# Performance work log

Hardware: AMD Instinct MI355X
Metric: run time of the kernel (lower is better)

## Reference

```python
import jax, jax.numpy as jnp
import numpy as np

N, E, R, H = 50000, 400000, 3, 3
IN, HID, OUT, C, B = 128, 64, 64, 16, 8


def _deg_norm(idx):
    # DGL GraphConv norm='both': deg.clamp(min=1) ** -0.5
    deg = jax.ops.segment_sum(jnp.ones(idx.shape, jnp.float32), idx, N)
    return jnp.maximum(deg, 1.0) ** -0.5


def _graph_conv(h, W, b, s, d):
    # h: [N, ..., F_in]; norm by src out-degree, matmul, scatter-sum to dst, norm by dst in-degree
    ns, nd = _deg_norm(s), _deg_norm(d)
    bshape = (N,) + (1,) * (h.ndim - 1)
    hw = (h * ns.reshape(bshape)) @ W
    agg = jax.ops.segment_sum(hw[s], d, N)
    return agg * nd.reshape(bshape) + b


def _gat(h, W, al, ar, b, s, d):
    # h: [N, HID] -> [N, H, HID] multi-head GAT with edge softmax over incoming edges
    f = (h @ W).reshape(N, H, HID)
    el = jnp.sum(f * al, axis=-1)  # [N, H]
    er = jnp.sum(f * ar, axis=-1)  # [N, H]
    e = jax.nn.leaky_relu(el[s] + er[d], 0.2)  # [E, H]
    m = jax.ops.segment_max(e, d, N)
    ez = jnp.exp(e - m[d])
    z = jax.ops.segment_sum(ez, d, N)
    alpha = ez / (z[d] + 1e-9)  # [E, H]
    out = jax.ops.segment_sum(alpha[:, :, None] * f[s], d, N)  # [N, H, HID]
    return out + b.reshape(H, HID)


def setup_inputs() -> dict:
    key = jax.random.key(0)
    k = jax.random.split(key, 12)
    s = 0.05
    return {
        "x": jax.random.normal(k[0], (N, IN), jnp.float32),
        "src": jax.random.randint(k[1], (R, E), 0, N, jnp.int32),
        "dst": jax.random.randint(k[2], (R, E), 0, N, jnp.int32),
        "graph_id": (jnp.arange(N, dtype=jnp.int32) * B // N).astype(jnp.int32),
        "W1": jax.random.normal(k[3], (R, IN, HID), jnp.float32) * s,
        "b1": jnp.zeros((R, HID), jnp.float32),
        "Wg": jax.random.normal(k[4], (R, HID, H * HID), jnp.float32) * s,
        "al": jax.random.normal(k[5], (R, H, HID), jnp.float32) * s,
        "ar": jax.random.normal(k[6], (R, H, HID), jnp.float32) * s,
        "bg": jnp.zeros((R, H * HID), jnp.float32),
        "W2": jax.random.normal(k[7], (R, HID, OUT), jnp.float32) * s,
        "b2": jnp.zeros((R, OUT), jnp.float32),
        "Wc": jax.random.normal(k[8], (OUT, C), jnp.float32) * s,
        "bc": jnp.zeros((C,), jnp.float32),
    }


def reference(x, src, dst, graph_id, W1, b1, Wg, al, ar, bg, W2, b2, Wc, bc):
    # conv1: per-relation GraphConv, aggregate='sum'
    h = sum(_graph_conv(x, W1[r], b1[r], src[r], dst[r]) for r in range(R))  # [N, HID]
    # F.normalize (L2 over dim=1, eps=1e-12)
    h = h / jnp.maximum(jnp.linalg.norm(h, axis=1, keepdims=True), 1e-12)
    # gatconv: per-relation GAT (3 heads), aggregate='sum'
    h = sum(_gat(h, Wg[r], al[r], ar[r], bg[r], src[r], dst[r]) for r in range(R))  # [N, H, HID]
    h = jax.nn.relu(h)
    # dropout(0.3) omitted: deterministic eval reference
    # conv2: GraphConv applied per head
    h = sum(_graph_conv(h, W2[r], b2[r], src[r], dst[r]) for r in range(R))  # [N, H, OUT]
    h = jax.nn.sigmoid(h)
    # dgl.mean_nodes over batched graphs
    cnt = jax.ops.segment_sum(jnp.ones((N,), jnp.float32), graph_id, B)
    pooled = jax.ops.segment_sum(h, graph_id, B) / jnp.maximum(cnt, 1.0)[:, None, None]  # [B, H, OUT]
    hg = jax.nn.sigmoid(pooled @ Wc + bc)  # [B, H, C]
    return jnp.mean(hg, axis=2)  # [B, H]
```

## Files before the change

kernel.cpp:

```cpp
#include <hip/hip_runtime.h>
#include <math.h>

#define NN 50000
#define EE 400000
#define RR 3
#define NH 3
#define FIN 128
#define HID 64
#define FOUT 64
#define NC 16
#define NB 8
#define NGAT 208

#define NBLK 32
#define CHK (EE / NBLK)
#define NRNG 4
#define RNGSZ (NN / NRNG)

typedef __attribute__((ext_vector_type(8))) short v8s;
typedef __attribute__((ext_vector_type(4))) float v4f;
typedef unsigned short u16;
typedef unsigned char u8;
typedef unsigned int u32;
typedef __attribute__((ext_vector_type(4))) unsigned short u16x4;

#define QS 32.0f
#define IQS (1.0f / 32.0f)

__device__ __forceinline__ u16 f2b(float f) {
  unsigned u = __float_as_uint(f);
  return (u16)((u + 0x7fffu + ((u >> 16) & 1u)) >> 16);
}
__device__ __forceinline__ float b2f(u16 b) {
  return __uint_as_float(((unsigned)b) << 16);
}
__device__ __forceinline__ float wexp(float e) {
  e = e > 0.f ? e : 0.2f * e;
  return __expf(e);
}
__device__ __forceinline__ u8 f2e(float v) {
  return (u8)(__builtin_amdgcn_cvt_pk_fp8_f32(v, 0.f, 0, false) & 0xff);
}

__global__ __launch_bounds__(1024) void k_hist(const int* __restrict__ src,
                                               const int* __restrict__ dst,
                                               u16* __restrict__ ps,
                                               u16* __restrict__ pd,
                                               u16* __restrict__ rank) {
  __shared__ u32 h[RNGSZ];
  int b = blockIdx.x;
  int kind = blockIdx.y >> 2, range = blockIdx.y & 3;
  int r = blockIdx.z;
  int lo = range * RNGSZ;
  for (int i = threadIdx.x; i < RNGSZ; i += 1024) h[i] = 0;
  __syncthreads();
  int base = r * EE + b * CHK;
  if (kind) {
    for (int i = threadIdx.x; i < CHK; i += 1024) {
      int d = dst[base + i] - lo;
      if ((unsigned)d < RNGSZ) rank[base + i] = (u16)atomicAdd(&h[d], 1u);
    }
  } else {
    for (int i = threadIdx.x; i < CHK; i += 1024) {
      int s = src[base + i] - lo;
      if ((unsigned)s < RNGSZ) atomicAdd(&h[s], 1u);
    }
  }
  __syncthreads();
  u16* p = (kind ? pd : ps) + (size_t)(r * NBLK + b) * NN + lo;
  for (int i = threadIdx.x; i < RNGSZ; i += 1024) p[i] = (u16)h[i];
}

__global__ void k_red(const u16* __restrict__ ps, const u16* __restrict__ pd,
                      int* __restrict__ degd, float* __restrict__ ns,
                      float* __restrict__ nd, u16* __restrict__ bpfx) {
  int i = blockIdx.x * 256 + threadIdx.x;
  if (i >= RR * NN) return;
  int r = i / NN, n = i - r * NN;
  u32 ss = 0, sd = 0;
  for (int b = 0; b < NBLK; ++b) {
    size_t o = (size_t)(r * NBLK + b) * NN + n;
    ss += ps[o];
    bpfx[o] = (u16)sd;
    sd += pd[o];
  }
  degd[i] = (int)sd;
  ns[i] = 1.0f / sqrtf((float)(ss > 1 ? ss : 1));
  nd[i] = 1.0f / sqrtf((float)(sd > 1 ? sd : 1));
}

__global__ void k_scan1(const int* __restrict__ deg, int* __restrict__ offs,
                        int* __restrict__ bsum) {
  __shared__ int sh[256];
  int gid = blockIdx.x * 256 + threadIdx.x;
  int v = (gid < RR * NN) ? deg[gid] : 0;
  sh[threadIdx.x] = v;
  __syncthreads();
  for (int off = 1; off < 256; off <<= 1) {
    int t = (threadIdx.x >= off) ? sh[threadIdx.x - off] : 0;
    __syncthreads();
    sh[threadIdx.x] += t;
    __syncthreads();
  }
  if (gid < RR * NN) offs[gid] = sh[threadIdx.x] - v;
  if (threadIdx.x == 255) bsum[blockIdx.x] = sh[255];
}

__global__ void k_scan2(int* __restrict__ bsum, int nb) {
  __shared__ int sh[1024];
  int v = (threadIdx.x < nb) ? bsum[threadIdx.x] : 0;
  sh[threadIdx.x] = v;
  __syncthreads();
  for (int off = 1; off < 1024; off <<= 1) {
    int t = (threadIdx.x >= off) ? sh[threadIdx.x - off] : 0;
    __syncthreads();
    sh[threadIdx.x] += t;
    __syncthreads();
  }
  if (threadIdx.x < nb) bsum[threadIdx.x] = sh[threadIdx.x] - v;
}

__global__ void k_scan3(int* __restrict__ offs, const int* __restrict__ bsum) {
  int i = blockIdx.x * 256 + threadIdx.x;
  if (i >= RR * NN) return;
  offs[i] = offs[i] + bsum[i / 256];
}

__global__ __launch_bounds__(1024) void k_place(const int* __restrict__ src,
                                                const int* __restrict__ dst,
                                                const int* __restrict__ offs,
                                                const u16* __restrict__ bpfx,
                                                const u16* __restrict__ rank,
                                                int* __restrict__ esrc) {
  int b = blockIdx.x;
  int range = blockIdx.y;
  int r = blockIdx.z;
  int lo = range * RNGSZ;
  int base = r * EE + b * CHK;
  for (int i = threadIdx.x; i < CHK; i += 1024) {
    int d = dst[base + i] - lo;
    if ((unsigned)d < RNGSZ) {
      int dg = d + lo;
      size_t o = (size_t)(r * NBLK + b) * NN + dg;
      int pos = offs[r * NN + dg] + (int)bpfx[o] + (int)rank[base + i];
      esrc[pos] = src[base + i];
    }
  }
}

__global__ void k_cast(const float4* __restrict__ in, u16x4* __restrict__ out, int n4) {
  int i = blockIdx.x * 256 + threadIdx.x;
  if (i >= n4) return;
  float4 v = in[i];
  u16x4 o;
  o.x = f2b(v.x); o.y = f2b(v.y); o.z = f2b(v.z); o.w = f2b(v.w);
  out[i] = o;
}

__global__ void k_bcomp(const float* __restrict__ Wg, const float* __restrict__ al,
                        const float* __restrict__ ar, float* __restrict__ B) {
  int i = blockIdx.x * 256 + threadIdx.x;
  if (i >= RR * HID * NGAT) return;
  int col = i % NGAT;
  int k = (i / NGAT) % HID;
  int r = i / (NGAT * HID);
  float v = 0.f;
  if (col < NH * HID) {
    v = Wg[((size_t)(r * HID + k)) * (NH * HID) + col];
  } else if (col < NH * HID + 6) {
    int c2 = col - NH * HID;
    int isar = c2 / NH, h = c2 % NH;
    const float* wg = Wg + ((size_t)(r * HID + k)) * (NH * HID) + h * HID;
    const float* av = (isar ? ar : al) + (r * NH + h) * HID;
    float a = 0.f;
#pragma unroll 8
    for (int c = 0; c < HID; ++c) a += wg[c] * av[c];
    v = a;
  }
  B[i] = v;
}

template <int K, int N, int OUTMODE>
__global__ __launch_bounds__(256) void k_gemm(const u16* __restrict__ A, int lda,
                                              const float* __restrict__ B0, int bstr,
                                              void* __restrict__ C0,
                                              u16* __restrict__ elr,
                                              const float* __restrict__ s0, int M) {
  constexpr int KP = K + 8;
  __shared__ __align__(16) u16 Bt[N * KP];
  int y = blockIdx.y;
  int rrel = (OUTMODE == 3) ? y / NH : y;
  int head = (OUTMODE == 3) ? y % NH : 0;
  const float* B = B0 + (size_t)rrel * bstr;
  const float* scale = s0 + (size_t)rrel * NN;
  const u16* Ab = A + head * HID;
  for (int i = threadIdx.x; i < K * N; i += 256) {
    int k = i / N, n = i % N;
    Bt[n * KP + k] = f2b(B[(size_t)k * N + n]);
  }
  __syncthreads();
  int wid = threadIdx.x >> 6, lane = threadIdx.x & 63;
  int l15 = lane & 15, lg = lane >> 4;
  constexpr int NT = N / 16;
  int ntiles = (M + 63) >> 6;
  for (int tile = blockIdx.x; tile < ntiles; tile += gridDim.x) {
    int mbase = tile * 64 + wid * 16;
    v4f acc[NT];
#pragma unroll
    for (int t = 0; t < NT; ++t) acc[t] = (v4f)(0.f);
    int arow = mbase + l15;
    if (arow >= M) arow = M - 1;
    const u16* ap = Ab + (size_t)arow * lda + lg * 8;
#pragma unroll
    for (int ks = 0; ks < K / 32; ++ks) {
      v8s a = *(const v8s*)(ap + ks * 32);
#pragma unroll
      for (int t = 0; t < NT; ++t) {
        v8s b = *(const v8s*)(&Bt[(t * 16 + l15) * KP + lg * 8 + ks * 32]);
        acc[t] = __builtin_amdgcn_mfma_f32_16x16x32_bf16(a, b, acc[t], 0, 0, 0);
      }
    }
#pragma unroll
    for (int q = 0; q < 4; ++q) {
      int row = mbase + lg * 4 + q;
      if (row >= M) continue;
      if (OUTMODE == 1) {
        float s = scale[row] * QS;
        u8* C = (u8*)C0 + ((size_t)y * M + row) * 64;
#pragma unroll
        for (int t = 0; t < NT; ++t) C[t * 16 + l15] = f2e(acc[t][q] * s);
      } else if (OUTMODE == 2) {
        u32* C = (u32*)C0 + ((size_t)y * M + row) * 64;
#pragma unroll
        for (int tm = 0; tm < 4; ++tm) {
          u32 pk = __builtin_amdgcn_cvt_pk_fp8_f32(acc[tm][q] * QS,
                                                   acc[tm + 4][q] * QS, 0, false);
          pk = __builtin_amdgcn_cvt_pk_fp8_f32(acc[tm + 8][q] * QS, 0.f, pk, true);
          C[tm * 16 + l15] = pk;
        }
        if (l15 < 6)
          elr[((size_t)y * M + row) * 8 + (l15 < 3 ? l15 : l15 + 1)] =
              f2b(acc[12][q]);
      } else {
        float s = scale[row] * QS;
        u8* C = (u8*)C0 + (((size_t)rrel * M + row) * 64) * 4 + head;
#pragma unroll
        for (int t = 0; t < NT; ++t) C[(t * 16 + l15) * 4] = f2e(acc[t][q] * s);
      }
    }
  }
}

__global__ void k_g1(const int* __restrict__ offs, const int* __restrict__ degd,
                     const int* __restrict__ esrc, const u8* __restrict__ c1pk,
                     const float* __restrict__ nd, const float* __restrict__ b1,
                     u16* __restrict__ h1b) {
  int node = blockIdx.x * 4 + (threadIdx.x >> 6);
  int lane = threadIdx.x & 63;
  if (node >= NN) return;
  float v = 0.f;
#pragma unroll
  for (int r = 0; r < RR; ++r) {
    int start = offs[r * NN + node];
    int deg = degd[r * NN + node];
    const u8* base = c1pk + (size_t)r * NN * 64 + lane;
    float t = 0.f;
    int j = 0;
    for (; j + 4 <= deg; j += 4) {
      int s0 = esrc[start + j], s1 = esrc[start + j + 1];
      int s2 = esrc[start + j + 2], s3 = esrc[start + j + 3];
      float a0 = __builtin_amdgcn_cvt_f32_fp8((u32)base[(size_t)s0 * 64], 0);
      float a1 = __builtin_amdgcn_cvt_f32_fp8((u32)base[(size_t)s1 * 64], 0);
      float a2 = __builtin_amdgcn_cvt_f32_fp8((u32)base[(size_t)s2 * 64], 0);
      float a3 = __builtin_amdgcn_cvt_f32_fp8((u32)base[(size_t)s3 * 64], 0);
      t += (a0 + a1) + (a2 + a3);
    }
    for (; j < deg; ++j)
      t += __builtin_amdgcn_cvt_f32_fp8((u32)base[(size_t)esrc[start + j] * 64], 0);
    v += t * nd[r * NN + node];
  }
  v = v * IQS + b1[lane] + b1[HID + lane] + b1[2 * HID + lane];
  float sq = v * v;
  for (int off = 32; off; off >>= 1) sq += __shfl_xor(sq, off);
  float nrm = sqrtf(sq);
  nrm = nrm > 1e-12f ? nrm : 1e-12f;
  h1b[node * HID + lane] = f2b(v / nrm);
}

__global__ void k_ew(const int* __restrict__ offs, const int* __restrict__ degd,
                     const int* __restrict__ esrc, const u16* __restrict__ elr,
                     u16* __restrict__ ew) {
  int i = blockIdx.x * 256 + threadIdx.x;
  if (i >= RR * NN) return;
  int r = i / NN;
  int start = offs[i], deg = degd[i];
  const u16* ed = elr + (size_t)i * 8 + 4;
  float e0 = b2f(ed[0]), e1 = b2f(ed[1]), e2 = b2f(ed[2]);
  for (int j = 0; j < deg; ++j) {
    int s = esrc[start + j];
    const u16* es = elr + ((size_t)r * NN + s) * 8;
    u16x4 o;
    o.x = f2b(wexp(b2f(es[0]) + e0));
    o.y = f2b(wexp(b2f(es[1]) + e1));
    o.z = f2b(wexp(b2f(es[2]) + e2));
    o.w = 0;
    *(u16x4*)(ew + (size_t)(start + j) * 4) = o;
  }
}

__global__ void k_gatg(const int* __restrict__ offs, const int* __restrict__ degd,
                       const int* __restrict__ esrc, const u32* __restrict__ fpk,
                       const u16* __restrict__ ew, const float* __restrict__ bg,
                       u16* __restrict__ gatb) {
  int node = blockIdx.x * 4 + (threadIdx.x >> 6);
  int lane = threadIdx.x & 63;
  if (node >= NN) return;
  float o0 = 0.f, o1 = 0.f, o2 = 0.f;
#pragma unroll
  for (int r = 0; r < RR; ++r) {
    const u32* f = fpk + (size_t)r * NN * 64 + lane;
    int start = offs[r * NN + node];
    int deg = degd[r * NN + node];
    float z0 = 0.f, z1 = 0.f, z2 = 0.f;
    float a0 = 0.f, a1 = 0.f, a2 = 0.f;
    int j = 0;
    for (; j + 4 <= deg; j += 4) {
      int p = start + j;
      int s0 = esrc[p], s1 = esrc[p + 1], s2 = esrc[p + 2], s3 = esrc[p + 3];
      u16x4 wa = *(const u16x4*)(ew + (size_t)p * 4);
      u16x4 wb = *(const u16x4*)(ew + (size_t)(p + 1) * 4);
      u16x4 wc = *(const u16x4*)(ew + (size_t)(p + 2) * 4);
      u16x4 wd = *(const u16x4*)(ew + (size_t)(p + 3) * 4);
      u32 v0 = f[(size_t)s0 * 64];
      u32 v1 = f[(size_t)s1 * 64];
      u32 v2 = f[(size_t)s2 * 64];
      u32 v3 = f[(size_t)s3 * 64];
      float w;
      w = b2f(wa.x); z0 += w; a0 += w * __builtin_amdgcn_cvt_f32_fp8(v0, 0);
      w = b2f(wa.y); z1 += w; a1 += w * __builtin_amdgcn_cvt_f32_fp8(v0, 1);
      w = b2f(wa.z); z2 += w; a2 += w * __builtin_amdgcn_cvt_f32_fp8(v0, 2);
      w = b2f(wb.x); z0 += w; a0 += w * __builtin_amdgcn_cvt_f32_fp8(v1, 0);
      w = b2f(wb.y); z1 += w; a1 += w * __builtin_amdgcn_cvt_f32_fp8(v1, 1);
      w = b2f(wb.z); z2 += w; a2 += w * __builtin_amdgcn_cvt_f32_fp8(v1, 2);
      w = b2f(wc.x); z0 += w; a0 += w * __builtin_amdgcn_cvt_f32_fp8(v2, 0);
      w = b2f(wc.y); z1 += w; a1 += w * __builtin_amdgcn_cvt_f32_fp8(v2, 1);
      w = b2f(wc.z); z2 += w; a2 += w * __builtin_amdgcn_cvt_f32_fp8(v2, 2);
      w = b2f(wd.x); z0 += w; a0 += w * __builtin_amdgcn_cvt_f32_fp8(v3, 0);
      w = b2f(wd.y); z1 += w; a1 += w * __builtin_amdgcn_cvt_f32_fp8(v3, 1);
      w = b2f(wd.z); z2 += w; a2 += w * __builtin_amdgcn_cvt_f32_fp8(v3, 2);
    }
    for (; j < deg; ++j) {
      int p = start + j;
      u16x4 wa = *(const u16x4*)(ew + (size_t)p * 4);
      u32 v0 = f[(size_t)esrc[p] * 64];
      float w;
      w = b2f(wa.x); z0 += w; a0 += w * __builtin_amdgcn_cvt_f32_fp8(v0, 0);
      w = b2f(wa.y); z1 += w; a1 += w * __builtin_amdgcn_cvt_f32_fp8(v0, 1);
      w = b2f(wa.z); z2 += w; a2 += w * __builtin_amdgcn_cvt_f32_fp8(v0, 2);
    }
    o0 += a0 / (z0 + 1e-9f);
    o1 += a1 / (z1 + 1e-9f);
    o2 += a2 / (z2 + 1e-9f);
  }
  float ov[NH] = {o0, o1, o2};
#pragma unroll
  for (int h = 0; h < NH; ++h) {
    int j = h * HID + lane;
    float v = ov[h] * IQS + bg[j] + bg[NH * HID + j] + bg[2 * NH * HID + j];
    gatb[(size_t)node * (NH * HID) + j] = f2b(fmaxf(v, 0.f));
  }
}

__global__ void k_g2(const int* __restrict__ offs, const int* __restrict__ degd,
                     const int* __restrict__ esrc, const u32* __restrict__ c2pk,
                     const float* __restrict__ nd, const float* __restrict__ b2,
                     u16* __restrict__ agg2b) {
  int node = blockIdx.x * 4 + (threadIdx.x >> 6);
  int lane = threadIdx.x & 63;
  if (node >= NN) return;
  float o0 = 0.f, o1 = 0.f, o2 = 0.f;
#pragma unroll
  for (int r = 0; r < RR; ++r) {
    const u32* hw = c2pk + (size_t)r * NN * 64 + lane;
    int start = offs[r * NN + node];
    int deg = degd[r * NN + node];
    float a0 = 0.f, a1 = 0.f, a2 = 0.f;
    int j = 0;
    for (; j + 4 <= deg; j += 4) {
      int p = start + j;
      u32 v0 = hw[(size_t)esrc[p] * 64];
      u32 v1 = hw[(size_t)esrc[p + 1] * 64];
      u32 v2 = hw[(size_t)esrc[p + 2] * 64];
      u32 v3 = hw[(size_t)esrc[p + 3] * 64];
      a0 += (__builtin_amdgcn_cvt_f32_fp8(v0, 0) + __builtin_amdgcn_cvt_f32_fp8(v1, 0)) +
            (__builtin_amdgcn_cvt_f32_fp8(v2, 0) + __builtin_amdgcn_cvt_f32_fp8(v3, 0));
      a1 += (__builtin_amdgcn_cvt_f32_fp8(v0, 1) + __builtin_amdgcn_cvt_f32_fp8(v1, 1)) +
            (__builtin_amdgcn_cvt_f32_fp8(v2, 1) + __builtin_amdgcn_cvt_f32_fp8(v3, 1));
      a2 += (__builtin_amdgcn_cvt_f32_fp8(v0, 2) + __builtin_amdgcn_cvt_f32_fp8(v1, 2)) +
            (__builtin_amdgcn_cvt_f32_fp8(v2, 2) + __builtin_amdgcn_cvt_f32_fp8(v3, 2));
    }
    for (; j < deg; ++j) {
      u32 v0 = hw[(size_t)esrc[start + j] * 64];
      a0 += __builtin_amdgcn_cvt_f32_fp8(v0, 0);
      a1 += __builtin_amdgcn_cvt_f32_fp8(v0, 1);
      a2 += __builtin_amdgcn_cvt_f32_fp8(v0, 2);
    }
    float ndv = nd[r * NN + node];
    o0 += a0 * ndv; o1 += a1 * ndv; o2 += a2 * ndv;
  }
  float b2s = b2[lane] + b2[FOUT + lane] + b2[2 * FOUT + lane];
  float ov[NH] = {o0, o1, o2};
#pragma unroll
  for (int h = 0; h < NH; ++h) {
    float v = 1.0f / (1.0f + __expf(-(ov[h] * IQS + b2s)));
    agg2b[(size_t)node * (NH * FOUT) + h * FOUT + lane] = f2b(v);
  }
}

__global__ void k_cnt2(const int* __restrict__ gid, float* __restrict__ cnt) {
  __shared__ int loc[NB];
  if (threadIdx.x < NB) loc[threadIdx.x] = 0;
  __syncthreads();
  int i = blockIdx.x * 256 + threadIdx.x;
  if (i < NN) atomicAdd(&loc[gid[i]], 1);
  __syncthreads();
  if (threadIdx.x < NB) atomicAdd(&cnt[threadIdx.x], (float)loc[threadIdx.x]);
}

__global__ void k_pool(const u16* __restrict__ h3, const int* __restrict__ gid,
                       float* __restrict__ pooled) {
  int j = threadIdx.x;
  int start = blockIdx.x * 128;
  if (start >= NN) return;
  int end = start + 128;
  if (end > NN) end = NN;
  int gcur = gid[start];
  float acc = 0.f;
  for (int n = start; n < end; ++n) {
    int g = gid[n];
    if (g != gcur) {
      atomicAdd(&pooled[gcur * (NH * FOUT) + j], acc);
      acc = 0.f;
      gcur = g;
    }
    acc += b2f(h3[(size_t)n * (NH * FOUT) + j]);
  }
  atomicAdd(&pooled[gcur * (NH * FOUT) + j], acc);
}

__global__ void k_final(const float* __restrict__ pooled, const float* __restrict__ cnt,
                        const float* __restrict__ Wc, const float* __restrict__ bc,
                        float* __restrict__ out) {
  int t = threadIdx.x;
  if (t >= NB * NH) return;
  int b = t / NH;
  float inv = 1.0f / fmaxf(cnt[b], 1.0f);
  const float* p = pooled + t * FOUT;
  float sacc = 0.f;
  for (int c = 0; c < NC; ++c) {
    float acc = bc[c];
    for (int o = 0; o < FOUT; ++o) acc += p[o] * inv * Wc[o * NC + c];
    sacc += 1.0f / (1.0f + __expf(-acc));
  }
  out[t] = sacc * (1.0f / NC);
}

extern "C" void kernel_launch(void* const* d_in, const int* in_sizes, int n_in,
                              void* d_out, int out_size, void* d_ws, size_t ws_size,
                              hipStream_t stream) {
  const float* x = (const float*)d_in[0];
  const int* src = (const int*)d_in[1];
  const int* dst = (const int*)d_in[2];
  const int* gid = (const int*)d_in[3];
  const float* W1 = (const float*)d_in[4];
  const float* b1 = (const float*)d_in[5];
  const float* Wg = (const float*)d_in[6];
  const float* al = (const float*)d_in[7];
  const float* ar = (const float*)d_in[8];
  const float* bg = (const float*)d_in[9];
  const float* W2 = (const float*)d_in[10];
  const float* b2 = (const float*)d_in[11];
  const float* Wc = (const float*)d_in[12];
  const float* bc = (const float*)d_in[13];
  float* out = (float*)d_out;

  float* cnt = (float*)d_ws;
  float* pooled = cnt + NB;
  size_t zero_bytes = ((size_t)NB + NB * NH * FOUT) * 4;
  int* degd = (int*)(pooled + NB * NH * FOUT);
  int* offs = degd + RR * NN;
  int* bsum = offs + RR * NN + 8;
  int* esrc = bsum + 1024;
  float* ns = (float*)(esrc + (size_t)RR * EE);
  float* nd = ns + RR * NN;
  float* Bcomp = nd + RR * NN;
  u16* elr = (u16*)(Bcomp + RR * HID * NGAT);
  u16* ew = elr + (size_t)RR * NN * 8;
  u16* xb = ew + (size_t)RR * EE * 4;
  u16* h1b = xb + (size_t)NN * FIN;
  u8* c1pk = (u8*)(h1b + (size_t)NN * HID);
  u16* gatb = (u16*)(c1pk + (size_t)RR * NN * 64);
  u32* fpk = (u32*)(gatb + (size_t)NN * NH * HID);
  u32* c2pk = fpk;
  u16* agg2b = xb;
  u16* ps = (u16*)fpk;
  u16* pd = ps + (size_t)RR * NBLK * NN;
  u16* bpfx = pd + (size_t)RR * NBLK * NN;
  u16* rank = bpfx + (size_t)RR * NBLK * NN;

  hipMemsetAsync(d_ws, 0, zero_bytes, stream);

  const int nscan = RR * NN;
  const int nblk1 = (nscan + 255) / 256;

  k_hist<<<dim3(NBLK, 8, RR), 1024, 0, stream>>>(src, dst, ps, pd, rank);
  k_red<<<nblk1, 256, 0, stream>>>(ps, pd, degd, ns, nd, bpfx);
  k_scan1<<<nblk1, 256, 0, stream>>>(degd, offs, bsum);
  k_scan2<<<1, 1024, 0, stream>>>(bsum, nblk1);
  k_scan3<<<nblk1, 256, 0, stream>>>(offs, bsum);
  k_place<<<dim3(NBLK, NRNG, RR), 1024, 0, stream>>>(src, dst, offs, bpfx, rank, esrc);

  k_cast<<<(NN * FIN / 4 + 255) / 256, 256, 0, stream>>>((const float4*)x, (u16x4*)xb,
                                                         NN * FIN / 4);
  k_bcomp<<<(RR * HID * NGAT + 255) / 256, 256, 0, stream>>>(Wg, al, ar, Bcomp);

  k_gemm<FIN, HID, 1><<<dim3(782, RR), 256, 0, stream>>>(
      xb, FIN, W1, FIN * HID, c1pk, nullptr, ns, NN);
  k_g1<<<(NN + 3) / 4, 256, 0, stream>>>(offs, degd, esrc, c1pk, nd, b1, h1b);

  k_gemm<HID, NGAT, 2><<<dim3(782, RR), 256, 0, stream>>>(
      h1b, HID, Bcomp, HID * NGAT, fpk, elr, ns, NN);
  k_ew<<<nblk1, 256, 0, stream>>>(offs, degd, esrc, elr, ew);
  k_gatg<<<(NN + 3) / 4, 256, 0, stream>>>(offs, degd, esrc, fpk, ew, bg, gatb);

  k_gemm<HID, FOUT, 3><<<dim3(782, RR * NH), 256, 0, stream>>>(
      gatb, NH * HID, W2, HID * FOUT, c2pk, nullptr, ns, NN);
  k_g2<<<(NN + 3) / 4, 256, 0, stream>>>(offs, degd, esrc, c2pk, nd, b2, agg2b);

  k_cnt2<<<(NN + 255) / 256, 256, 0, stream>>>(gid, cnt);
  k_pool<<<(NN + 127) / 128, 192, 0, stream>>>(agg2b, gid, pooled);
  k_final<<<1, 64, 0, stream>>>(pooled, cnt, Wc, bc, out);
}
```

Before: 552.8 us.

## Reorder GAT and conv2 to aggregate before matmul, stacking relations into one GEMM

The GAT layer now gathers the 64-wide normalized features (fp8) per edge, weighted by softmax coefficients normalized in a separate edge pass. The head projection then runs afterwards as a single GEMM over stacked per-relation aggregates (K=192). conv2 likewise aggregates the 64-wide per-head features before one stacked GEMM, with bias and sigmoid fused into its epilogue. This cuts gather width and removes the large per-relation GAT projection. In exchange it adds a second exp pass over edges and a larger intermediate aggregate buffer that is written and then read back by the GEMMs.

```diff
diff --git a/kernel.cpp b/kernel.cpp
--- a/kernel.cpp
+++ b/kernel.cpp
@@ -10,7 +10,6 @@
 #define FOUT 64
 #define NC 16
 #define NB 8
-#define NGAT 208
 
 #define NBLK 32
 #define CHK (EE / NBLK)
@@ -157,19 +156,16 @@
   out[i] = o;
 }
 
-__global__ void k_bcomp(const float* __restrict__ Wg, const float* __restrict__ al,
-                        const float* __restrict__ ar, float* __restrict__ B) {
-  int i = blockIdx.x * 256 + threadIdx.x;
-  if (i >= RR * HID * NGAT) return;
-  int col = i % NGAT;
-  int k = (i / NGAT) % HID;
-  int r = i / (NGAT * HID);
+__global__ void k_wel(const float* __restrict__ Wg, const float* __restrict__ al,
+                      const float* __restrict__ ar, float* __restrict__ Bel) {
+  int i = blockIdx.x * 256 + threadIdx.x;
+  if (i >= RR * HID * 16) return;
+  int col = i & 15;
+  int k = (i >> 4) % HID;
+  int r = i / (16 * HID);
   float v = 0.f;
-  if (col < NH * HID) {
-    v = Wg[((size_t)(r * HID + k)) * (NH * HID) + col];
-  } else if (col < NH * HID + 6) {
-    int c2 = col - NH * HID;
-    int isar = c2 / NH, h = c2 % NH;
+  if (col < 6) {
+    int isar = col / 3, h = col % 3;
     const float* wg = Wg + ((size_t)(r * HID + k)) * (NH * HID) + h * HID;
     const float* av = (isar ? ar : al) + (r * NH + h) * HID;
     float a = 0.f;
@@ -177,23 +173,48 @@
     for (int c = 0; c < HID; ++c) a += wg[c] * av[c];
     v = a;
   }
-  B[i] = v;
+  Bel[i] = v;
+}
+
+__global__ void k_wstack(const float* __restrict__ Wg, const float* __restrict__ W2,
+                         const float* __restrict__ bg, const float* __restrict__ b2,
+                         float* __restrict__ Bg, float* __restrict__ B2s,
+                         float* __restrict__ bgs, float* __restrict__ b2s) {
+  int i = blockIdx.x * 256 + threadIdx.x;
+  const int NG = RR * 192 * 64;
+  const int N2 = 192 * 64;
+  if (i < NG) {
+    int o = i & 63;
+    int rk = (i >> 6) % 192;
+    int h = i / (192 * 64);
+    int r = rk >> 6, k = rk & 63;
+    Bg[i] = Wg[((size_t)(r * HID + k)) * (NH * HID) + h * HID + o];
+  } else if (i < NG + N2) {
+    int j = i - NG;
+    int o = j & 63;
+    int rk = j >> 6;
+    int r = rk >> 6, k = rk & 63;
+    B2s[j] = W2[((size_t)(r * HID + k)) * FOUT + o];
+  } else if (i < NG + N2 + 192) {
+    int j = i - NG - N2;
+    bgs[j] = bg[j] + bg[192 + j] + bg[384 + j];
+  } else if (i < NG + N2 + 192 + 64) {
+    int j = i - NG - N2 - 192;
+    b2s[j] = b2[j] + b2[64 + j] + b2[128 + j];
+  }
 }
 
 template <int K, int N, int OUTMODE>
 __global__ __launch_bounds__(256) void k_gemm(const u16* __restrict__ A, int lda,
                                               const float* __restrict__ B0, int bstr,
                                               void* __restrict__ C0,
-                                              u16* __restrict__ elr,
+                                              const float* __restrict__ bias,
                                               const float* __restrict__ s0, int M) {
   constexpr int KP = K + 8;
   __shared__ __align__(16) u16 Bt[N * KP];
   int y = blockIdx.y;
-  int rrel = (OUTMODE == 3) ? y / NH : y;
-  int head = (OUTMODE == 3) ? y % NH : 0;
-  const float* B = B0 + (size_t)rrel * bstr;
-  const float* scale = s0 + (size_t)rrel * NN;
-  const u16* Ab = A + head * HID;
+  const float* B = B0 + (size_t)y * bstr;
+  const u16* Ab = (OUTMODE == 5 || OUTMODE == 6) ? A + y * 192 : A;
   for (int i = threadIdx.x; i < K * N; i += 256) {
     int k = i / N, n = i % N;
     Bt[n * KP + k] = f2b(B[(size_t)k * N + n]);
@@ -225,27 +246,28 @@
       int row = mbase + lg * 4 + q;
       if (row >= M) continue;
       if (OUTMODE == 1) {
-        float s = scale[row] * QS;
+        float s = s0[(size_t)y * NN + row] * QS;
         u8* C = (u8*)C0 + ((size_t)y * M + row) * 64;
 #pragma unroll
         for (int t = 0; t < NT; ++t) C[t * 16 + l15] = f2e(acc[t][q] * s);
-      } else if (OUTMODE == 2) {
-        u32* C = (u32*)C0 + ((size_t)y * M + row) * 64;
-#pragma unroll
-        for (int tm = 0; tm < 4; ++tm) {
-          u32 pk = __builtin_amdgcn_cvt_pk_fp8_f32(acc[tm][q] * QS,
-                                                   acc[tm + 4][q] * QS, 0, false);
-          pk = __builtin_amdgcn_cvt_pk_fp8_f32(acc[tm + 8][q] * QS, 0.f, pk, true);
-          C[tm * 16 + l15] = pk;
+      } else if (OUTMODE == 4) {
+        if (l15 < 6)
+          ((u16*)C0)[((size_t)y * M + row) * 8 + (l15 < 3 ? l15 : l15 + 1)] =
+              f2b(acc[0][q]);
+      } else if (OUTMODE == 5) {
+        u8* C = (u8*)C0 + (size_t)row * 192 + y * 64;
+#pragma unroll
+        for (int t = 0; t < NT; ++t) {
+          float v = acc[t][q] * IQS + bias[y * 64 + t * 16 + l15];
+          C[t * 16 + l15] = f2e(fmaxf(v, 0.f) * QS);
         }
-        if (l15 < 6)
-          elr[((size_t)y * M + row) * 8 + (l15 < 3 ? l15 : l15 + 1)] =
-              f2b(acc[12][q]);
       } else {
-        float s = scale[row] * QS;
-        u8* C = (u8*)C0 + (((size_t)rrel * M + row) * 64) * 4 + head;
-#pragma unroll
-        for (int t = 0; t < NT; ++t) C[(t * 16 + l15) * 4] = f2e(acc[t][q] * s);
+        u16* C = (u16*)C0 + (size_t)row * 192 + y * 64;
+#pragma unroll
+        for (int t = 0; t < NT; ++t) {
+          float v = acc[t][q] * IQS + bias[t * 16 + l15];
+          C[t * 16 + l15] = f2b(1.0f / (1.0f + __expf(-v)));
+        }
       }
     }
   }
@@ -254,7 +276,7 @@
 __global__ void k_g1(const int* __restrict__ offs, const int* __restrict__ degd,
                      const int* __restrict__ esrc, const u8* __restrict__ c1pk,
                      const float* __restrict__ nd, const float* __restrict__ b1,
-                     u16* __restrict__ h1b) {
+                     u16* __restrict__ h1b, u8* __restrict__ h1q) {
   int node = blockIdx.x * 4 + (threadIdx.x >> 6);
   int lane = threadIdx.x & 63;
   if (node >= NN) return;
@@ -284,44 +306,52 @@
   for (int off = 32; off; off >>= 1) sq += __shfl_xor(sq, off);
   float nrm = sqrtf(sq);
   nrm = nrm > 1e-12f ? nrm : 1e-12f;
-  h1b[node * HID + lane] = f2b(v / nrm);
-}
-
-__global__ void k_ew(const int* __restrict__ offs, const int* __restrict__ degd,
-                     const int* __restrict__ esrc, const u16* __restrict__ elr,
-                     u16* __restrict__ ew) {
+  float hv = v / nrm;
+  h1b[node * HID + lane] = f2b(hv);
+  h1q[node * HID + lane] = f2e(hv * QS);
+}
+
+__global__ void k_ew2(const int* __restrict__ offs, const int* __restrict__ degd,
+                      const int* __restrict__ esrc, const u16* __restrict__ elr,
+                      u16* __restrict__ ew) {
   int i = blockIdx.x * 256 + threadIdx.x;
   if (i >= RR * NN) return;
   int r = i / NN;
   int start = offs[i], deg = degd[i];
   const u16* ed = elr + (size_t)i * 8 + 4;
   float e0 = b2f(ed[0]), e1 = b2f(ed[1]), e2 = b2f(ed[2]);
+  float z0 = 0.f, z1 = 0.f, z2 = 0.f;
+  for (int j = 0; j < deg; ++j) {
+    int s = esrc[start + j];
+    const u16* es = elr + ((size_t)r * NN + s) * 8;
+    z0 += wexp(b2f(es[0]) + e0);
+    z1 += wexp(b2f(es[1]) + e1);
+    z2 += wexp(b2f(es[2]) + e2);
+  }
+  float i0 = 1.f / (z0 + 1e-9f), i1 = 1.f / (z1 + 1e-9f), i2 = 1.f / (z2 + 1e-9f);
   for (int j = 0; j < deg; ++j) {
     int s = esrc[start + j];
     const u16* es = elr + ((size_t)r * NN + s) * 8;
     u16x4 o;
-    o.x = f2b(wexp(b2f(es[0]) + e0));
-    o.y = f2b(wexp(b2f(es[1]) + e1));
-    o.z = f2b(wexp(b2f(es[2]) + e2));
+    o.x = f2b(wexp(b2f(es[0]) + e0) * i0);
+    o.y = f2b(wexp(b2f(es[1]) + e1) * i1);
+    o.z = f2b(wexp(b2f(es[2]) + e2) * i2);
     o.w = 0;
     *(u16x4*)(ew + (size_t)(start + j) * 4) = o;
   }
 }
 
-__global__ void k_gatg(const int* __restrict__ offs, const int* __restrict__ degd,
-                       const int* __restrict__ esrc, const u32* __restrict__ fpk,
-                       const u16* __restrict__ ew, const float* __restrict__ bg,
-                       u16* __restrict__ gatb) {
+__global__ void k_gatg2(const int* __restrict__ offs, const int* __restrict__ degd,
+                        const int* __restrict__ esrc, const u8* __restrict__ h1q,
+                        const u16* __restrict__ ew, u16* __restrict__ agg) {
   int node = blockIdx.x * 4 + (threadIdx.x >> 6);
   int lane = threadIdx.x & 63;
   if (node >= NN) return;
-  float o0 = 0.f, o1 = 0.f, o2 = 0.f;
+  const u8* base = h1q + lane;
 #pragma unroll
   for (int r = 0; r < RR; ++r) {
-    const u32* f = fpk + (size_t)r * NN * 64 + lane;
     int start = offs[r * NN + node];
     int deg = degd[r * NN + node];
-    float z0 = 0.f, z1 = 0.f, z2 = 0.f;
     float a0 = 0.f, a1 = 0.f, a2 = 0.f;
     int j = 0;
     for (; j + 4 <= deg; j += 4) {
@@ -331,89 +361,70 @@
       u16x4 wb = *(const u16x4*)(ew + (size_t)(p + 1) * 4);
       u16x4 wc = *(const u16x4*)(ew + (size_t)(p + 2) * 4);
       u16x4 wd = *(const u16x4*)(ew + (size_t)(p + 3) * 4);
-      u32 v0 = f[(size_t)s0 * 64];
-      u32 v1 = f[(size_t)s1 * 64];
-      u32 v2 = f[(size_t)s2 * 64];
-      u32 v3 = f[(size_t)s3 * 64];
-      float w;
-      w = b2f(wa.x); z0 += w; a0 += w * __builtin_amdgcn_cvt_f32_fp8(v0, 0);
-      w = b2f(wa.y); z1 += w; a1 += w * __builtin_amdgcn_cvt_f32_fp8(v0, 1);
-      w = b2f(wa.z); z2 += w; a2 += w * __builtin_amdgcn_cvt_f32_fp8(v0, 2);
-      w = b2f(wb.x); z0 += w; a0 += w * __builtin_amdgcn_cvt_f32_fp8(v1, 0);
-      w = b2f(wb.y); z1 += w; a1 += w * __builtin_amdgcn_cvt_f32_fp8(v1, 1);
-      w = b2f(wb.z); z2 += w; a2 += w * __builtin_amdgcn_cvt_f32_fp8(v1, 2);
-      w = b2f(wc.x); z0 += w; a0 += w * __builtin_amdgcn_cvt_f32_fp8(v2, 0);
-      w = b2f(wc.y); z1 += w; a1 += w * __builtin_amdgcn_cvt_f32_fp8(v2, 1);
-      w = b2f(wc.z); z2 += w; a2 += w * __builtin_amdgcn_cvt_f32_fp8(v2, 2);
-      w = b2f(wd.x); z0 += w; a0 += w * __builtin_amdgcn_cvt_f32_fp8(v3, 0);
-      w = b2f(wd.y); z1 += w; a1 += w * __builtin_amdgcn_cvt_f32_fp8(v3, 1);
-      w = b2f(wd.z); z2 += w; a2 += w * __builtin_amdgcn_cvt_f32_fp8(v3, 2);
+      float v0 = __builtin_amdgcn_cvt_f32_fp8((u32)base[(size_t)s0 * 64], 0);
+      float v1 = __builtin_amdgcn_cvt_f32_fp8((u32)base[(size_t)s1 * 64], 0);
+      float v2 = __builtin_amdgcn_cvt_f32_fp8((u32)base[(size_t)s2 * 64], 0);
+      float v3 = __builtin_amdgcn_cvt_f32_fp8((u32)base[(size_t)s3 * 64], 0);
+      a0 += b2f(wa.x) * v0 + b2f(wb.x) * v1 + b2f(wc.x) * v2 + b2f(wd.x) * v3;
+      a1 += b2f(wa.y) * v0 + b2f(wb.y) * v1 + b2f(wc.y) * v2 + b2f(wd.y) * v3;
+      a2 += b2f(wa.z) * v0 + b2f(wb.z) * v1 + b2f(wc.z) * v2 + b2f(wd.z) * v3;
     }
     for (; j < deg; ++j) {
       int p = start + j;
       u16x4 wa = *(const u16x4*)(ew + (size_t)p * 4);
-      u32 v0 = f[(size_t)esrc[p] * 64];
-      float w;
-      w = b2f(wa.x); z0 += w; a0 += w * __builtin_amdgcn_cvt_f32_fp8(v0, 0);
-      w = b2f(wa.y); z1 += w; a1 += w * __builtin_amdgcn_cvt_f32_fp8(v0, 1);
-      w = b2f(wa.z); z2 += w; a2 += w * __builtin_amdgcn_cvt_f32_fp8(v0, 2);
-    }
-    o0 += a0 / (z0 + 1e-9f);
-    o1 += a1 / (z1 + 1e-9f);
-    o2 += a2 / (z2 + 1e-9f);
-  }
-  float ov[NH] = {o0, o1, o2};
-#pragma unroll
-  for (int h = 0; h < NH; ++h) {
-    int j = h * HID + lane;
-    float v = ov[h] * IQS + bg[j] + bg[NH * HID + j] + bg[2 * NH * HID + j];
-    gatb[(size_t)node * (NH * HID) + j] = f2b(fmaxf(v, 0.f));
-  }
-}
-
-__global__ void k_g2(const int* __restrict__ offs, const int* __restrict__ degd,
-                     const int* __restrict__ esrc, const u32* __restrict__ c2pk,
-                     const float* __restrict__ nd, const float* __restrict__ b2,
-                     u16* __restrict__ agg2b) {
+      float v = __builtin_amdgcn_cvt_f32_fp8((u32)base[(size_t)esrc[p] * 64], 0);
+      a0 += b2f(wa.x) * v;
+      a1 += b2f(wa.y) * v;
+      a2 += b2f(wa.z) * v;
+    }
+    size_t ob = (size_t)node * 576 + r * 64 + lane;
+    agg[ob] = f2b(a0);
+    agg[ob + 192] = f2b(a1);
+    agg[ob + 384] = f2b(a2);
+  }
+}
+
+__global__ void k_g22(const int* __restrict__ offs, const int* __restrict__ degd,
+                      const int* __restrict__ esrc, const u8* __restrict__ gq,
+                      const float* __restrict__ ns, const float* __restrict__ nd,
+                      u16* __restrict__ agg) {
   int node = blockIdx.x * 4 + (threadIdx.x >> 6);
   int lane = threadIdx.x & 63;
   if (node >= NN) return;
-  float o0 = 0.f, o1 = 0.f, o2 = 0.f;
+  const u8* g0 = gq + lane;
+  const u8* g1 = gq + 64 + lane;
+  const u8* g2 = gq + 128 + lane;
 #pragma unroll
   for (int r = 0; r < RR; ++r) {
-    const u32* hw = c2pk + (size_t)r * NN * 64 + lane;
     int start = offs[r * NN + node];
     int deg = degd[r * NN + node];
+    const float* nsr = ns + (size_t)r * NN;
     float a0 = 0.f, a1 = 0.f, a2 = 0.f;
     int j = 0;
-    for (; j + 4 <= deg; j += 4) {
-      int p = start + j;
-      u32 v0 = hw[(size_t)esrc[p] * 64];
-      u32 v1 = hw[(size_t)esrc[p + 1] * 64];
-      u32 v2 = hw[(size_t)esrc[p + 2] * 64];
-      u32 v3 = hw[(size_t)esrc[p + 3] * 64];
-      a0 += (__builtin_amdgcn_cvt_f32_fp8(v0, 0) + __builtin_amdgcn_cvt_f32_fp8(v1, 0)) +
-            (__builtin_amdgcn_cvt_f32_fp8(v2, 0) + __builtin_amdgcn_cvt_f32_fp8(v3, 0));
-      a1 += (__builtin_amdgcn_cvt_f32_fp8(v0, 1) + __builtin_amdgcn_cvt_f32_fp8(v1, 1)) +
-            (__builtin_amdgcn_cvt_f32_fp8(v2, 1) + __builtin_amdgcn_cvt_f32_fp8(v3, 1));
-      a2 += (__builtin_amdgcn_cvt_f32_fp8(v0, 2) + __builtin_amdgcn_cvt_f32_fp8(v1, 2)) +
-            (__builtin_amdgcn_cvt_f32_fp8(v2, 2) + __builtin_amdgcn_cvt_f32_fp8(v3, 2));
-    }
-    for (; j < deg; ++j) {
-      u32 v0 = hw[(size_t)esrc[start + j] * 64];
-      a0 += __builtin_amdgcn_cvt_f32_fp8(v0, 0);
-      a1 += __builtin_amdgcn_cvt_f32_fp8(v0, 1);
-      a2 += __builtin_amdgcn_cvt_f32_fp8(v0, 2);
+    for (; j + 2 <= deg; j += 2) {
+      int s0 = esrc[start + j], s1 = esrc[start + j + 1];
+      float w0 = nsr[s0], w1 = nsr[s1];
+      size_t o0 = (size_t)s0 * 192, o1 = (size_t)s1 * 192;
+      a0 += w0 * __builtin_amdgcn_cvt_f32_fp8((u32)g0[o0], 0) +
+            w1 * __builtin_amdgcn_cvt_f32_fp8((u32)g0[o1], 0);
+      a1 += w0 * __builtin_amdgcn_cvt_f32_fp8((u32)g1[o0], 0) +
+            w1 * __builtin_amdgcn_cvt_f32_fp8((u32)g1[o1], 0);
+      a2 += w0 * __builtin_amdgcn_cvt_f32_fp8((u32)g2[o0], 0) +
+            w1 * __builtin_amdgcn_cvt_f32_fp8((u32)g2[o1], 0);
+    }
+    if (j < deg) {
+      int s0 = esrc[start + j];
+      float w0 = nsr[s0];
+      size_t o0 = (size_t)s0 * 192;
+      a0 += w0 * __builtin_amdgcn_cvt_f32_fp8((u32)g0[o0], 0);
+      a1 += w0 * __builtin_amdgcn_cvt_f32_fp8((u32)g1[o0], 0);
+      a2 += w0 * __builtin_amdgcn_cvt_f32_fp8((u32)g2[o0], 0);
     }
     float ndv = nd[r * NN + node];
-    o0 += a0 * ndv; o1 += a1 * ndv; o2 += a2 * ndv;
-  }
-  float b2s = b2[lane] + b2[FOUT + lane] + b2[2 * FOUT + lane];
-  float ov[NH] = {o0, o1, o2};
-#pragma unroll
-  for (int h = 0; h < NH; ++h) {
-    float v = 1.0f / (1.0f + __expf(-(ov[h] * IQS + b2s)));
-    agg2b[(size_t)node * (NH * FOUT) + h * FOUT + lane] = f2b(v);
+    size_t ob = (size_t)node * 576 + r * 64 + lane;
+    agg[ob] = f2b(a0 * ndv);
+    agg[ob + 192] = f2b(a1 * ndv);
+    agg[ob + 384] = f2b(a2 * ndv);
   }
 }
 
@@ -493,17 +504,21 @@
   int* esrc = bsum + 1024;
   float* ns = (float*)(esrc + (size_t)RR * EE);
   float* nd = ns + RR * NN;
-  float* Bcomp = nd + RR * NN;
-  u16* elr = (u16*)(Bcomp + RR * HID * NGAT);
+  float* Bel = nd + RR * NN;
+  float* Bg = Bel + RR * HID * 16;
+  float* B2s = Bg + RR * 192 * 64;
+  float* bgs = B2s + 192 * 64;
+  float* b2s = bgs + 192;
+  u16* elr = (u16*)(b2s + 64);
   u16* ew = elr + (size_t)RR * NN * 8;
   u16* xb = ew + (size_t)RR * EE * 4;
   u16* h1b = xb + (size_t)NN * FIN;
-  u8* c1pk = (u8*)(h1b + (size_t)NN * HID);
-  u16* gatb = (u16*)(c1pk + (size_t)RR * NN * 64);
-  u32* fpk = (u32*)(gatb + (size_t)NN * NH * HID);
-  u32* c2pk = fpk;
+  u8* h1q = (u8*)(h1b + (size_t)NN * HID);
+  u8* c1pk = h1q + (size_t)NN * HID;
+  u8* gq = c1pk + (size_t)RR * NN * 64;
+  u16* agg = (u16*)(gq + (size_t)NN * 192);
   u16* agg2b = xb;
-  u16* ps = (u16*)fpk;
+  u16* ps = agg;
   u16* pd = ps + (size_t)RR * NBLK * NN;
   u16* bpfx = pd + (size_t)RR * NBLK * NN;
   u16* rank = bpfx + (size_t)RR * NBLK * NN;
@@ -522,20 +537,24 @@
 
   k_cast<<<(NN * FIN / 4 + 255) / 256, 256, 0, stream>>>((const float4*)x, (u16x4*)xb,
                                                          NN * FIN / 4);
-  k_bcomp<<<(RR * HID * NGAT + 255) / 256, 256, 0, stream>>>(Wg, al, ar, Bcomp);
+  k_wel<<<(RR * HID * 16 + 255) / 256, 256, 0, stream>>>(Wg, al, ar, Bel);
+  k_wstack<<<(RR * 192 * 64 + 192 * 64 + 256 + 255) / 256, 256, 0, stream>>>(
+      Wg, W2, bg, b2, Bg, B2s, bgs, b2s);
 
   k_gemm<FIN, HID, 1><<<dim3(782, RR), 256, 0, stream>>>(
       xb, FIN, W1, FIN * HID, c1pk, nullptr, ns, NN);
-  k_g1<<<(NN + 3) / 4, 256, 0, stream>>>(offs, degd, esrc, c1pk, nd, b1, h1b);
-
-  k_gemm<HID, NGAT, 2><<<dim3(782, RR), 256, 0, stream>>>(
-      h1b, HID, Bcomp, HID * NGAT, fpk, elr, ns, NN);
-  k_ew<<<nblk1, 256, 0, stream>>>(offs, degd, esrc, elr, ew);
-  k_gatg<<<(NN + 3) / 4, 256, 0, stream>>>(offs, degd, esrc, fpk, ew, bg, gatb);
-
-  k_gemm<HID, FOUT, 3><<<dim3(782, RR * NH), 256, 0, stream>>>(
-      gatb, NH * HID, W2, HID * FOUT, c2pk, nullptr, ns, NN);
-  k_g2<<<(NN + 3) / 4, 256, 0, stream>>>(offs, degd, esrc, c2pk, nd, b2, agg2b);
+  k_g1<<<(NN + 3) / 4, 256, 0, stream>>>(offs, degd, esrc, c1pk, nd, b1, h1b, h1q);
+
+  k_gemm<HID, 16, 4><<<dim3(782, RR), 256, 0, stream>>>(
+      h1b, HID, Bel, HID * 16, elr, nullptr, nullptr, NN);
+  k_ew2<<<nblk1, 256, 0, stream>>>(offs, degd, esrc, elr, ew);
+  k_gatg2<<<(NN + 3) / 4, 256, 0, stream>>>(offs, degd, esrc, h1q, ew, agg);
+  k_gemm<192, 64, 5><<<dim3(782, NH), 256, 0, stream>>>(
+      agg, 576, Bg, 192 * 64, gq, bgs, nullptr, NN);
+
+  k_g22<<<(NN + 3) / 4, 256, 0, stream>>>(offs, degd, esrc, gq, ns, nd, agg);
+  k_gemm<192, 64, 6><<<dim3(782, NH), 256, 0, stream>>>(
+      agg, 576, B2s, 0, agg2b, b2s, nullptr, NN);
 
   k_cnt2<<<(NN + 255) / 256, 256, 0, stream>>>(gid, cnt);
   k_pool<<<(NN + 127) / 128, 192, 0, stream>>>(agg2b, gid, pooled);
```

Result: no change. 549.8 us (-0.5%).
